# Kernel optimization log

Hardware: AMD Instinct MI355X
Metric: run time of the kernel (lower is better)

## Reference

```python
import jax, jax.numpy as jnp
import numpy as np

N = 32768
D = 256
NUM_POS = 4
TEMPS = 2
ID_NUM = N // TEMPS // NUM_POS  # 4096


def setup_inputs() -> dict:
    key = jax.random.key(0)
    k1, _ = jax.random.split(key)
    inputs = jax.random.normal(k1, (N, D), dtype=jnp.float32)
    # two modality halves, each half = each id repeated NUM_POS times
    targets = (jnp.arange(N, dtype=jnp.int64) // NUM_POS) % ID_NUM
    return {"inputs": inputs, "targets": targets}


def reference(inputs, targets):
    eps = 1e-6
    num_pos, temps = NUM_POS, TEMPS
    n = inputs.shape[0]
    id_num = n // temps // num_pos

    # centers: per-id mean (original python loop over ids == segment mean)
    ones = jnp.ones((n,), inputs.dtype)
    counts = jax.ops.segment_sum(ones, targets, num_segments=id_num)  # [id_num]
    centers = jax.ops.segment_sum(inputs, targets, num_segments=id_num) / counts[:, None]  # [id_num, D]

    # pairwise euclidean distance centers -> inputs  [id_num, N]
    d2 = (jnp.sum(centers * centers, axis=1)[:, None]
          + jnp.sum(inputs * inputs, axis=1)[None, :]
          - 2.0 * centers @ inputs.T)
    dist = jnp.sqrt(jnp.clip(d2, 1e-12, None))

    # is_neg_c2i: id of each center vs every sample
    center_ids = targets[jnp.arange(id_num) * num_pos]  # [id_num]
    is_neg = center_ids[:, None] != targets[None, :]    # [id_num, N]

    # negative mining (masked, fixed-shape version of an[an>1e-6].view)
    an = jnp.where(is_neg, dist, 0.0)
    valid_neg = an > eps
    n_neg = jnp.sum(valid_neg, axis=1).astype(dist.dtype)           # = N - temps*num_pos
    d_neg = jnp.sum(jnp.where(valid_neg, an, 0.0), axis=1) / n_neg  # per-center mean neg dist
    hard = valid_neg & (an < d_neg[:, None])                        # hard negatives (closer than mean)
    hard_cnt = jnp.sum(hard, axis=1).astype(dist.dtype)
    row_an = jnp.sum(jnp.where(hard, an, 0.0), axis=1) / hard_cnt   # per-center hard-neg mean
    an_mean = jnp.mean(row_an)

    # positives: center to its own samples
    ap = jnp.where(is_neg, 0.0, dist)
    valid_pos = ap > eps
    ap_mean = jnp.sum(jnp.where(valid_pos, ap, 0.0)) / jnp.sum(valid_pos).astype(dist.dtype)

    return ap_mean / an_mean
```

## Files before the change

### kernel.cpp

```cpp
#include <hip/hip_runtime.h>
#include <hip/hip_bf16.h>

#define NS   32768
#define DD   256
#define NPOS 4
#define IDN  4096

typedef __attribute__((ext_vector_type(8))) short short8;
typedef __attribute__((ext_vector_type(4))) float f32x4;

__device__ __forceinline__ unsigned short f2bf(float f) {
    unsigned int u = __builtin_bit_cast(unsigned int, f);
    unsigned int r = (u + 0x7FFFu + ((u >> 16) & 1u)) >> 16;
    return (unsigned short)r;
}

__device__ __forceinline__ void gload16(const void* g, void* lds) {
    __builtin_amdgcn_global_load_lds(
        (const __attribute__((address_space(1))) unsigned int*)g,
        (__attribute__((address_space(3))) unsigned int*)lds, 16, 0, 0);
}


__global__ void conv_k(const float* __restrict__ in, unsigned short* __restrict__ Xb,
                       float* __restrict__ x2) {
    int row  = blockIdx.x * 4 + (threadIdx.x >> 6);
    int lane = threadIdx.x & 63;
    const float4 v = *(const float4*)&in[(size_t)row * DD + lane * 4];
    ushort4 u;
    u.x = f2bf(v.x); u.y = f2bf(v.y); u.z = f2bf(v.z); u.w = f2bf(v.w);
    *(ushort4*)&Xb[(size_t)row * DD + lane * 4] = u;
    float sq = v.x * v.x + v.y * v.y + v.z * v.z + v.w * v.w;
    #pragma unroll
    for (int m = 1; m < 64; m <<= 1) sq += __shfl_xor(sq, m, 64);
    if (lane == 0) x2[row] = sq;
}

__global__ void centers_k(const float* __restrict__ in,
                          unsigned short* __restrict__ Cb, float* __restrict__ c2) {
    int r = blockIdx.x, d = threadIdx.x;
    const float* p0 = in + (size_t)(4 * r) * DD + d;
    const float* p1 = in + (size_t)(16384 + 4 * r) * DD + d;
    float s = 0.f;
    #pragma unroll
    for (int j = 0; j < 4; ++j) s += p0[(size_t)j * DD];
    #pragma unroll
    for (int j = 0; j < 4; ++j) s += p1[(size_t)j * DD];
    float mean = s * 0.125f;
    Cb[(size_t)r * DD + d] = f2bf(mean);
    float sq = mean * mean;
    #pragma unroll
    for (int m = 1; m < 64; m <<= 1) sq += __shfl_xor(sq, m, 64);
    __shared__ float sb[4];
    int lane = d & 63, w = d >> 6;
    if (lane == 0) sb[w] = sq;
    __syncthreads();
    if (d == 0) c2[r] = sb[0] + sb[1] + sb[2] + sb[3];
}

__global__ __launch_bounds__(256)
void pos_k(const float* __restrict__ in, const float* __restrict__ c2,
           const float* __restrict__ x2,
           float* __restrict__ possum, float* __restrict__ posdist) {
    const int r = blockIdx.x * 4 + (threadIdx.x >> 6);
    const int l = threadIdx.x & 63;
    float cx = 0.f, cy = 0.f, cz = 0.f, cw = 0.f;
    #pragma unroll
    for (int j = 0; j < 8; ++j) {
        const int rr = (j < 4) ? (4 * r + j) : (16384 + 4 * r + (j - 4));
        const float4 v = *(const float4*)&in[(size_t)rr * DD + l * 4];
        cx += v.x; cy += v.y; cz += v.z; cw += v.w;
    }
    cx *= 0.125f; cy *= 0.125f; cz *= 0.125f; cw *= 0.125f;
    const float c2v = c2[r];
    float ps = 0.f;
    #pragma unroll
    for (int j = 0; j < 8; ++j) {
        const int cc = (j < 4) ? (4 * r + j) : (16384 + 4 * r + (j - 4));
        const float4 xv = *(const float4*)&in[(size_t)cc * DD + l * 4];
        float p = cx * xv.x + cy * xv.y + cz * xv.z + cw * xv.w;
        #pragma unroll
        for (int m = 1; m < 64; m <<= 1) p += __shfl_xor(p, m, 64);
        float d2 = c2v + x2[cc] - 2.f * p;
        float dist = sqrtf(fmaxf(d2, 1e-12f));
        ps += dist;
        if (l == 0) posdist[r * 8 + j] = dist;
    }
    if (l == 0) possum[r] = ps;
}

__global__ void dneg_k(const float* __restrict__ negsum_all,
                       const float* __restrict__ possum,
                       const float* __restrict__ posdist,
                       float* __restrict__ dneg2,
                       float* __restrict__ pcs, float* __restrict__ pcc) {
    int r = blockIdx.x * 256 + threadIdx.x;
    if (r < IDN) {
        float dn = (negsum_all[r] - possum[r]) * (1.0f / 32760.0f);
        dneg2[r] = dn * dn;
        float s = 0.f, c = 0.f;
        #pragma unroll
        for (int j = 0; j < 8; ++j) {
            float d = posdist[r * 8 + j];
            if (d < dn) { s += d; c += 1.f; }
        }
        pcs[r] = s; pcc[r] = c;
    }
}


template <int PASS>
__global__ __launch_bounds__(512, 2)
void mpass_k(const unsigned short* __restrict__ Cb, const unsigned short* __restrict__ Xb,
             const float* __restrict__ c2, const float* __restrict__ x2,
             const float* __restrict__ dneg2,
             float* __restrict__ S, float* __restrict__ C) {
    __shared__ unsigned short As[64 * 512];
    __shared__ unsigned short Bs[2 * 32 * 512];

    const int tid = threadIdx.x;
    const int l  = tid & 63;
    const int w  = tid >> 6;
    const int wr = w >> 2;
    const int wc = w & 3;
    const int lr = l & 15;
    const int lc = l >> 4;
    const int bid = blockIdx.x;
    const int ch = bid & 7;
    const int bm = bid >> 3;
    const int colbase = ch * 4096;

    const unsigned short* bj[4]; unsigned int bslot[4];
    #pragma unroll
    for (int j = 0; j < 4; ++j) {
        const int s = w * 4 + j;
        const int kk2s = s >> 4;
        const int cbs  = s & 15;
        bj[j] = Xb + (size_t)(colbase + cbs * 16 + lr) * DD + kk2s * 32 + lc * 8;
        bslot[j] = (unsigned)(kk2s * 16 + cbs) * 512;
    }

    {
        const unsigned short* asrc = Cb + (size_t)(bm * 128 + lr) * DD + w * 32 + lc * 8;
        #pragma unroll
        for (int rb = 0; rb < 8; ++rb)
            gload16(asrc + (size_t)rb * 16 * DD, &As[(w * 8 + rb) * 512]);
        #pragma unroll
        for (int j = 0; j < 4; ++j)
            gload16(bj[j], &Bs[bslot[j]]);
    }
    __syncthreads();

    const int gr0 = bm * 128 + wr * 64;
    float c2v[16]; float dnv[16];
    #pragma unroll
    for (int mf = 0; mf < 4; ++mf)
        #pragma unroll
        for (int r = 0; r < 4; ++r) {
            const int row = gr0 + mf * 16 + lc * 4 + r;
            c2v[mf * 4 + r] = c2[row];
            dnv[mf * 4 + r] = (PASS == 2) ? dneg2[row] : 0.f;
        }

    float rs[16], rc[16];
    #pragma unroll
    for (int i = 0; i < 16; ++i) { rs[i] = 0.f; rc[i] = 0.f; }

    for (int step = 0; step < 16; ++step) {
        float x2v[4];
        #pragma unroll
        for (int nf = 0; nf < 4; ++nf)
            x2v[nf] = x2[colbase + step * 256 + wc * 64 + nf * 16 + lr];

        f32x4 acc[4][4];
        #pragma unroll
        for (int a = 0; a < 4; ++a)
            #pragma unroll
            for (int b = 0; b < 4; ++b) acc[a][b] = (f32x4){0.f, 0.f, 0.f, 0.f};

        #pragma unroll
        for (int ss = 0; ss < 4; ++ss) {
            const int g  = step * 4 + ss;
            const int gn = (g + 1) & 63;
            {
                const size_t go = (size_t)(gn >> 2) * (256 * DD) + (gn & 3) * 64;
                const unsigned int doff = (unsigned)(gn & 1) * 16384;
                #pragma unroll
                for (int j = 0; j < 4; ++j)
                    gload16(bj[j] + go, &Bs[doff + bslot[j]]);
            }
            const unsigned int boff = (unsigned)(g & 1) * 16384;
            #pragma unroll
            for (int kk2 = 0; kk2 < 2; ++kk2) {
                const int kkg = ss * 2 + kk2;
                short8 af[4], bf[4];
                #pragma unroll
                for (int mf = 0; mf < 4; ++mf)
                    af[mf] = *(const short8*)&As[((kkg * 8) + wr * 4 + mf) * 512 + l * 8];
                #pragma unroll
                for (int nf = 0; nf < 4; ++nf)
                    bf[nf] = *(const short8*)&Bs[boff + (kk2 * 16 + wc * 4 + nf) * 512 + l * 8];
                __builtin_amdgcn_s_setprio(1);
                #pragma unroll
                for (int mf = 0; mf < 4; ++mf)
                    #pragma unroll
                    for (int nf = 0; nf < 4; ++nf)
                        acc[mf][nf] = __builtin_amdgcn_mfma_f32_16x16x32_bf16(
                            af[mf], bf[nf], acc[mf][nf], 0, 0, 0);
                __builtin_amdgcn_s_setprio(0);
            }
            __syncthreads();
        }

        #pragma unroll
        for (int mf = 0; mf < 4; ++mf)
            #pragma unroll
            for (int nf = 0; nf < 4; ++nf)
                #pragma unroll
                for (int r = 0; r < 4; ++r) {
                    const int i = mf * 4 + r;
                    float d2 = fmaf(-2.f, acc[mf][nf][r], c2v[i] + x2v[nf]);
                    float d2c = fmaxf(d2, 1e-12f);
                    float dist = __builtin_amdgcn_sqrtf(d2c);
                    if (PASS == 1) {
                        rs[i] += dist;
                    } else {
                        bool h = d2c < dnv[i];
                        rs[i] += h ? dist : 0.f;
                        rc[i] += h ? 1.f : 0.f;
                    }
                }
    }

    #pragma unroll
    for (int i = 0; i < 16; ++i) {
        #pragma unroll
        for (int m = 1; m < 16; m <<= 1) {
            rs[i] += __shfl_xor(rs[i], m, 64);
            if (PASS == 2) rc[i] += __shfl_xor(rc[i], m, 64);
        }
    }
    if (lr == 0) {
        #pragma unroll
        for (int mf = 0; mf < 4; ++mf)
            #pragma unroll
            for (int r = 0; r < 4; ++r) {
                const int row = gr0 + mf * 16 + lc * 4 + r;
                atomicAdd(&S[row], rs[mf * 4 + r]);
                if (PASS == 2) atomicAdd(&C[row], rc[mf * 4 + r]);
            }
    }
}

__global__ void final_k(const float* __restrict__ hardsum,
                        const float* __restrict__ hardcnt,
                        const float* __restrict__ pcs, const float* __restrict__ pcc,
                        const float* __restrict__ possum, float* out) {
    float s_an = 0.f, s_ap = 0.f;
    for (int r = threadIdx.x; r < IDN; r += 256) {
        s_an += (hardsum[r] - pcs[r]) / fmaxf(hardcnt[r] - pcc[r], 1.0f);
        s_ap += possum[r];
    }
    #pragma unroll
    for (int m = 1; m < 64; m <<= 1) {
        s_an += __shfl_xor(s_an, m, 64);
        s_ap += __shfl_xor(s_ap, m, 64);
    }
    __shared__ float sb[8];
    int lane = threadIdx.x & 63, w = threadIdx.x >> 6;
    if (lane == 0) { sb[w] = s_an; sb[4 + w] = s_ap; }
    __syncthreads();
    if (threadIdx.x == 0) {
        float an = (sb[0] + sb[1] + sb[2] + sb[3]) / (float)IDN;
        float ap = (sb[4] + sb[5] + sb[6] + sb[7]) / (float)NS;
        out[0] = ap / an;
    }
}


extern "C" void kernel_launch(void* const* d_in, const int* in_sizes, int n_in,
                              void* d_out, int out_size, void* d_ws, size_t ws_size,
                              hipStream_t stream) {
    const float* inputs = (const float*)d_in[0];
    float* out = (float*)d_out;

    char* p = (char*)d_ws;
    unsigned short* Xb = (unsigned short*)p;  p += (size_t)NS * DD * 2;
    unsigned short* Cb = (unsigned short*)p;  p += (size_t)IDN * DD * 2;
    float* x2      = (float*)p;  p += (size_t)NS * 4;
    float* c2      = (float*)p;  p += (size_t)IDN * 4;
    float* dneg2   = (float*)p;  p += (size_t)IDN * 4;
    float* possum  = (float*)p;  p += (size_t)IDN * 4;
    float* posdist = (float*)p;  p += (size_t)IDN * 8 * 4;
    float* pcs     = (float*)p;  p += (size_t)IDN * 4;
    float* pcc     = (float*)p;  p += (size_t)IDN * 4;
    char* zp = p;
    float* negsum  = (float*)p;  p += (size_t)IDN * 4;
    float* hardsum = (float*)p;  p += (size_t)IDN * 4;
    float* hardcnt = (float*)p;  p += (size_t)IDN * 4;

    hipMemsetAsync(zp, 0, (size_t)(p - zp), stream);
    conv_k<<<NS / 4, 256, 0, stream>>>(inputs, Xb, x2);
    centers_k<<<IDN, 256, 0, stream>>>(inputs, Cb, c2);
    pos_k<<<IDN / 4, 256, 0, stream>>>(inputs, c2, x2, possum, posdist);

    mpass_k<1><<<256, 512, 0, stream>>>(Cb, Xb, c2, x2, dneg2, negsum, nullptr);
    dneg_k<<<IDN / 256, 256, 0, stream>>>(negsum, possum, posdist, dneg2, pcs, pcc);
    mpass_k<2><<<256, 512, 0, stream>>>(Cb, Xb, c2, x2, dneg2, hardsum, hardcnt);
    final_k<<<1, 256, 0, stream>>>(hardsum, hardcnt, pcs, pcc, possum, out);
}
```

Before: 278.0 us.

## Materialize fp16 squared distances in pass one and read them for hard-negative pass

The first matmul pass now optionally writes all clamped squared distances as fp16 into a large workspace buffer. A new streaming kernel then reads them to compute the hard-negative sums and counts, instead of recomputing the full bf16 GEMM in a second pass. This trades a second GEMM for a 256 MB write plus read of HBM, and it adds fp16 rounding to the threshold comparison. It falls back to the old recompute path if the workspace is too small.

```diff
diff --git a/kernel.cpp b/kernel.cpp
--- a/kernel.cpp
+++ b/kernel.cpp
@@ -13,6 +13,15 @@
     unsigned int u = __builtin_bit_cast(unsigned int, f);
     unsigned int r = (u + 0x7FFFu + ((u >> 16) & 1u)) >> 16;
     return (unsigned short)r;
+}
+
+__device__ __forceinline__ unsigned short f2h(float f) {
+    _Float16 h = (_Float16)f;
+    return __builtin_bit_cast(unsigned short, h);
+}
+__device__ __forceinline__ float h2f(unsigned short u) {
+    _Float16 h = __builtin_bit_cast(_Float16, u);
+    return (float)h;
 }
 
 __device__ __forceinline__ void gload16(const void* g, void* lds) {
@@ -109,12 +118,11 @@
 }
 
 
-template <int PASS>
+template <bool STORE>
 __global__ __launch_bounds__(512, 2)
-void mpass_k(const unsigned short* __restrict__ Cb, const unsigned short* __restrict__ Xb,
-             const float* __restrict__ c2, const float* __restrict__ x2,
-             const float* __restrict__ dneg2,
-             float* __restrict__ S, float* __restrict__ C) {
+void mpass1_k(const unsigned short* __restrict__ Cb, const unsigned short* __restrict__ Xb,
+              const float* __restrict__ c2, const float* __restrict__ x2,
+              float* __restrict__ S, unsigned short* __restrict__ D2) {
     __shared__ unsigned short As[64 * 512];
     __shared__ unsigned short Bs[2 * 32 * 512];
 
@@ -152,19 +160,19 @@
     __syncthreads();
 
     const int gr0 = bm * 128 + wr * 64;
-    float c2v[16]; float dnv[16];
+    float c2v[16];
     #pragma unroll
     for (int mf = 0; mf < 4; ++mf)
         #pragma unroll
-        for (int r = 0; r < 4; ++r) {
-            const int row = gr0 + mf * 16 + lc * 4 + r;
-            c2v[mf * 4 + r] = c2[row];
-            dnv[mf * 4 + r] = (PASS == 2) ? dneg2[row] : 0.f;
-        }
-
-    float rs[16], rc[16];
-    #pragma unroll
-    for (int i = 0; i < 16; ++i) { rs[i] = 0.f; rc[i] = 0.f; }
+        for (int r = 0; r < 4; ++r)
+            c2v[mf * 4 + r] = c2[gr0 + mf * 16 + lc * 4 + r];
+
+    float rs[16];
+    #pragma unroll
+    for (int i = 0; i < 16; ++i) rs[i] = 0.f;
+
+    unsigned short* dbase = STORE ? (D2 + (size_t)bid * 524288 + (size_t)w * 256 + l * 4)
+                                  : nullptr;
 
     for (int step = 0; step < 16; ++step) {
         float x2v[4];
@@ -215,31 +223,209 @@
         #pragma unroll
         for (int mf = 0; mf < 4; ++mf)
             #pragma unroll
+            for (int r = 0; r < 4; ++r) {
+                const int i = mf * 4 + r;
+                float d2c[4];
+                #pragma unroll
+                for (int nf = 0; nf < 4; ++nf) {
+                    float d2 = fmaf(-2.f, acc[mf][nf][r], c2v[i] + x2v[nf]);
+                    d2c[nf] = fmaxf(d2, 1e-12f);
+                    rs[i] += __builtin_amdgcn_sqrtf(d2c[nf]);
+                }
+                if (STORE) {
+                    ushort4 pk;
+                    pk.x = f2h(d2c[0]); pk.y = f2h(d2c[1]);
+                    pk.z = f2h(d2c[2]); pk.w = f2h(d2c[3]);
+                    *(ushort4*)(dbase + (size_t)(step * 16 + i) * 2048) = pk;
+                }
+            }
+    }
+
+    #pragma unroll
+    for (int i = 0; i < 16; ++i)
+        #pragma unroll
+        for (int m = 1; m < 16; m <<= 1)
+            rs[i] += __shfl_xor(rs[i], m, 64);
+    if (lr == 0) {
+        #pragma unroll
+        for (int mf = 0; mf < 4; ++mf)
+            #pragma unroll
+            for (int r = 0; r < 4; ++r)
+                atomicAdd(&S[gr0 + mf * 16 + lc * 4 + r], rs[mf * 4 + r]);
+    }
+}
+
+__global__ __launch_bounds__(512)
+void hard_k(const unsigned short* __restrict__ D2, const float* __restrict__ dneg2,
+            float* __restrict__ S, float* __restrict__ C) {
+    const int tid = threadIdx.x;
+    const int l  = tid & 63;
+    const int w  = tid >> 6;
+    const int wr = w >> 2;
+    const int lc = l >> 4;
+    const int lr = l & 15;
+    const int bid2 = blockIdx.x;
+    const int obid = bid2 >> 2;
+    const int sub  = bid2 & 3;
+    const int bm = obid >> 3;
+    const int gr0 = bm * 128 + wr * 64;
+
+    float dnv[16];
+    #pragma unroll
+    for (int mf = 0; mf < 4; ++mf)
+        #pragma unroll
+        for (int r = 0; r < 4; ++r)
+            dnv[mf * 4 + r] = dneg2[gr0 + mf * 16 + lc * 4 + r];
+
+    float rs[16], rc[16];
+    #pragma unroll
+    for (int i = 0; i < 16; ++i) { rs[i] = 0.f; rc[i] = 0.f; }
+
+    const unsigned short* dbase = D2 + (size_t)obid * 524288 + (size_t)w * 256 + l * 4;
+
+    for (int s4 = 0; s4 < 4; ++s4) {
+        const int step = sub * 4 + s4;
+        #pragma unroll
+        for (int i = 0; i < 16; ++i) {
+            ushort4 pk = *(const ushort4*)(dbase + (size_t)(step * 16 + i) * 2048);
+            float d0 = h2f(pk.x), d1 = h2f(pk.y), d2 = h2f(pk.z), d3 = h2f(pk.w);
+            const float dn = dnv[i];
+            if (d0 < dn) { rs[i] += __builtin_amdgcn_sqrtf(d0); rc[i] += 1.f; }
+            if (d1 < dn) { rs[i] += __builtin_amdgcn_sqrtf(d1); rc[i] += 1.f; }
+            if (d2 < dn) { rs[i] += __builtin_amdgcn_sqrtf(d2); rc[i] += 1.f; }
+            if (d3 < dn) { rs[i] += __builtin_amdgcn_sqrtf(d3); rc[i] += 1.f; }
+        }
+    }
+
+    #pragma unroll
+    for (int i = 0; i < 16; ++i)
+        #pragma unroll
+        for (int m = 1; m < 16; m <<= 1) {
+            rs[i] += __shfl_xor(rs[i], m, 64);
+            rc[i] += __shfl_xor(rc[i], m, 64);
+        }
+    if (lr == 0) {
+        #pragma unroll
+        for (int mf = 0; mf < 4; ++mf)
+            #pragma unroll
+            for (int r = 0; r < 4; ++r) {
+                const int row = gr0 + mf * 16 + lc * 4 + r;
+                atomicAdd(&S[row], rs[mf * 4 + r]);
+                atomicAdd(&C[row], rc[mf * 4 + r]);
+            }
+    }
+}
+
+__global__ __launch_bounds__(512, 2)
+void mpass2_k(const unsigned short* __restrict__ Cb, const unsigned short* __restrict__ Xb,
+              const float* __restrict__ c2, const float* __restrict__ x2,
+              const float* __restrict__ dneg2,
+              float* __restrict__ S, float* __restrict__ C) {
+    __shared__ unsigned short As[64 * 512];
+    __shared__ unsigned short Bs[2 * 32 * 512];
+    const int tid = threadIdx.x;
+    const int l  = tid & 63;
+    const int w  = tid >> 6;
+    const int wr = w >> 2;
+    const int wc = w & 3;
+    const int lr = l & 15;
+    const int lc = l >> 4;
+    const int bid = blockIdx.x;
+    const int ch = bid & 7;
+    const int bm = bid >> 3;
+    const int colbase = ch * 4096;
+    const unsigned short* bj[4]; unsigned int bslot[4];
+    #pragma unroll
+    for (int j = 0; j < 4; ++j) {
+        const int s = w * 4 + j;
+        const int kk2s = s >> 4, cbs = s & 15;
+        bj[j] = Xb + (size_t)(colbase + cbs * 16 + lr) * DD + kk2s * 32 + lc * 8;
+        bslot[j] = (unsigned)(kk2s * 16 + cbs) * 512;
+    }
+    {
+        const unsigned short* asrc = Cb + (size_t)(bm * 128 + lr) * DD + w * 32 + lc * 8;
+        #pragma unroll
+        for (int rb = 0; rb < 8; ++rb)
+            gload16(asrc + (size_t)rb * 16 * DD, &As[(w * 8 + rb) * 512]);
+        #pragma unroll
+        for (int j = 0; j < 4; ++j) gload16(bj[j], &Bs[bslot[j]]);
+    }
+    __syncthreads();
+    const int gr0 = bm * 128 + wr * 64;
+    float c2v[16], dnv[16];
+    #pragma unroll
+    for (int mf = 0; mf < 4; ++mf)
+        #pragma unroll
+        for (int r = 0; r < 4; ++r) {
+            const int row = gr0 + mf * 16 + lc * 4 + r;
+            c2v[mf * 4 + r] = c2[row];
+            dnv[mf * 4 + r] = dneg2[row];
+        }
+    float rs[16], rc[16];
+    #pragma unroll
+    for (int i = 0; i < 16; ++i) { rs[i] = 0.f; rc[i] = 0.f; }
+    for (int step = 0; step < 16; ++step) {
+        float x2v[4];
+        #pragma unroll
+        for (int nf = 0; nf < 4; ++nf)
+            x2v[nf] = x2[colbase + step * 256 + wc * 64 + nf * 16 + lr];
+        f32x4 acc[4][4];
+        #pragma unroll
+        for (int a = 0; a < 4; ++a)
+            #pragma unroll
+            for (int b = 0; b < 4; ++b) acc[a][b] = (f32x4){0.f, 0.f, 0.f, 0.f};
+        #pragma unroll
+        for (int ss = 0; ss < 4; ++ss) {
+            const int g = step * 4 + ss, gn = (g + 1) & 63;
+            {
+                const size_t go = (size_t)(gn >> 2) * (256 * DD) + (gn & 3) * 64;
+                const unsigned int doff = (unsigned)(gn & 1) * 16384;
+                #pragma unroll
+                for (int j = 0; j < 4; ++j) gload16(bj[j] + go, &Bs[doff + bslot[j]]);
+            }
+            const unsigned int boff = (unsigned)(g & 1) * 16384;
+            #pragma unroll
+            for (int kk2 = 0; kk2 < 2; ++kk2) {
+                const int kkg = ss * 2 + kk2;
+                short8 af[4], bf[4];
+                #pragma unroll
+                for (int mf = 0; mf < 4; ++mf)
+                    af[mf] = *(const short8*)&As[((kkg * 8) + wr * 4 + mf) * 512 + l * 8];
+                #pragma unroll
+                for (int nf = 0; nf < 4; ++nf)
+                    bf[nf] = *(const short8*)&Bs[boff + (kk2 * 16 + wc * 4 + nf) * 512 + l * 8];
+                __builtin_amdgcn_s_setprio(1);
+                #pragma unroll
+                for (int mf = 0; mf < 4; ++mf)
+                    #pragma unroll
+                    for (int nf = 0; nf < 4; ++nf)
+                        acc[mf][nf] = __builtin_amdgcn_mfma_f32_16x16x32_bf16(
+                            af[mf], bf[nf], acc[mf][nf], 0, 0, 0);
+                __builtin_amdgcn_s_setprio(0);
+            }
+            __syncthreads();
+        }
+        #pragma unroll
+        for (int mf = 0; mf < 4; ++mf)
+            #pragma unroll
             for (int nf = 0; nf < 4; ++nf)
                 #pragma unroll
                 for (int r = 0; r < 4; ++r) {
                     const int i = mf * 4 + r;
                     float d2 = fmaf(-2.f, acc[mf][nf][r], c2v[i] + x2v[nf]);
                     float d2c = fmaxf(d2, 1e-12f);
-                    float dist = __builtin_amdgcn_sqrtf(d2c);
-                    if (PASS == 1) {
-                        rs[i] += dist;
-                    } else {
-                        bool h = d2c < dnv[i];
-                        rs[i] += h ? dist : 0.f;
-                        rc[i] += h ? 1.f : 0.f;
-                    }
+                    bool h = d2c < dnv[i];
+                    rs[i] += h ? __builtin_amdgcn_sqrtf(d2c) : 0.f;
+                    rc[i] += h ? 1.f : 0.f;
                 }
     }
-
-    #pragma unroll
-    for (int i = 0; i < 16; ++i) {
+    #pragma unroll
+    for (int i = 0; i < 16; ++i)
         #pragma unroll
         for (int m = 1; m < 16; m <<= 1) {
             rs[i] += __shfl_xor(rs[i], m, 64);
-            if (PASS == 2) rc[i] += __shfl_xor(rc[i], m, 64);
-        }
-    }
+            rc[i] += __shfl_xor(rc[i], m, 64);
+        }
     if (lr == 0) {
         #pragma unroll
         for (int mf = 0; mf < 4; ++mf)
@@ -247,7 +433,7 @@
             for (int r = 0; r < 4; ++r) {
                 const int row = gr0 + mf * 16 + lc * 4 + r;
                 atomicAdd(&S[row], rs[mf * 4 + r]);
-                if (PASS == 2) atomicAdd(&C[row], rc[mf * 4 + r]);
+                atomicAdd(&C[row], rc[mf * 4 + r]);
             }
     }
 }
@@ -298,14 +484,25 @@
     float* negsum  = (float*)p;  p += (size_t)IDN * 4;
     float* hardsum = (float*)p;  p += (size_t)IDN * 4;
     float* hardcnt = (float*)p;  p += (size_t)IDN * 4;
-
-    hipMemsetAsync(zp, 0, (size_t)(p - zp), stream);
+    p = (char*)(((size_t)p + 255) & ~(size_t)255);
+    unsigned short* D2 = (unsigned short*)p;
+    size_t required_big = (size_t)(p - (char*)d_ws) + (size_t)NS * IDN * 2;
+
+    const bool big = (ws_size >= required_big);
+
+    hipMemsetAsync(zp, 0, (size_t)(3 * IDN * 4), stream);
     conv_k<<<NS / 4, 256, 0, stream>>>(inputs, Xb, x2);
     centers_k<<<IDN, 256, 0, stream>>>(inputs, Cb, c2);
     pos_k<<<IDN / 4, 256, 0, stream>>>(inputs, c2, x2, possum, posdist);
 
-    mpass_k<1><<<256, 512, 0, stream>>>(Cb, Xb, c2, x2, dneg2, negsum, nullptr);
-    dneg_k<<<IDN / 256, 256, 0, stream>>>(negsum, possum, posdist, dneg2, pcs, pcc);
-    mpass_k<2><<<256, 512, 0, stream>>>(Cb, Xb, c2, x2, dneg2, hardsum, hardcnt);
+    if (big) {
+        mpass1_k<true><<<256, 512, 0, stream>>>(Cb, Xb, c2, x2, negsum, D2);
+        dneg_k<<<IDN / 256, 256, 0, stream>>>(negsum, possum, posdist, dneg2, pcs, pcc);
+        hard_k<<<1024, 512, 0, stream>>>(D2, dneg2, hardsum, hardcnt);
+    } else {
+        mpass1_k<false><<<256, 512, 0, stream>>>(Cb, Xb, c2, x2, negsum, nullptr);
+        dneg_k<<<IDN / 256, 256, 0, stream>>>(negsum, possum, posdist, dneg2, pcs, pcc);
+        mpass2_k<<<256, 512, 0, stream>>>(Cb, Xb, c2, x2, dneg2, hardsum, hardcnt);
+    }
     final_k<<<1, 256, 0, stream>>>(hardsum, hardcnt, pcs, pcc, possum, out);
 }
```

Result: no change. 278.9 us (+0.3%).
